# Optimization experiments

Measured on AMD Instinct MI355X. Metric: run time of the kernel, lower is better.

Reference implementation:

```python
import jax, jax.numpy as jnp
import numpy as np

N_NODES = 100000
N_EDGES = 800000
IN_SIZE = 256
OUT_SIZE = 256


def setup_inputs() -> dict:
    key = jax.random.key(0)
    k1, k2, k3, k4, k5, k6 = jax.random.split(key, 6)
    stdv = 1.0 / np.sqrt(OUT_SIZE)
    x = jax.random.normal(k1, (N_NODES, IN_SIZE), dtype=jnp.float32)
    weight = jax.random.uniform(k2, (IN_SIZE, OUT_SIZE), dtype=jnp.float32, minval=-stdv, maxval=stdv)
    bias = jax.random.uniform(k3, (1, OUT_SIZE), dtype=jnp.float32, minval=-stdv, maxval=stdv)
    edge_weight = jax.random.uniform(k4, (N_EDGES,), dtype=jnp.float32)
    edge_src = jax.random.randint(k5, (N_EDGES,), 0, N_NODES, dtype=jnp.int32)
    edge_dst = jax.random.randint(k6, (N_EDGES,), 0, N_NODES, dtype=jnp.int32)
    return {"x": x, "weight": weight, "bias": bias,
            "edge_weight": edge_weight, "edge_src": edge_src, "edge_dst": edge_dst}


def reference(x, weight, bias, edge_weight, edge_src, edge_dst):
    # supp = input @ W  (dense GEMM)
    supp = jnp.matmul(x, weight)  # [N, out]
    # out = spmm(A, supp): A in COO form -> gather source rows, scale, scatter-add to dst
    msgs = supp[edge_src] * edge_weight[:, None]  # [E, out]
    agg = jax.ops.segment_sum(msgs, edge_dst, num_segments=x.shape[0])  # [N, out]
    return agg + bias
```

## Files before the change

### kernel.cpp

```cpp
#include <hip/hip_runtime.h>
#include <hip/hip_bf16.h>

#define N_NODES 100000
#define N_EDGES 800000
#define K_DIM 256
#define N_DIM 256

typedef __attribute__((ext_vector_type(8)))  short  short8;
typedef __attribute__((ext_vector_type(4)))  float  f32x4;
typedef __attribute__((ext_vector_type(4)))  float  float4v;

__device__ short g_Wt[K_DIM * N_DIM];
__device__ int   g_bsums[512];
__device__ int   g_boff[512];

static __device__ inline short f32_to_bf16s(float f) {
    __bf16 h = (__bf16)f;
    return __builtin_bit_cast(short, h);
}

__global__ __launch_bounds__(256) void convert_w_kernel(const float* __restrict__ W) {
    const int n = blockIdx.x;
    const int k = threadIdx.x;
    g_Wt[n * K_DIM + k] = f32_to_bf16s(W[(size_t)k * N_DIM + n]);
}

__global__ __launch_bounds__(256) void mfma_gemm_kernel(const float* __restrict__ X,
                                                        float* __restrict__ S,
                                                        int M) {
    const int wave = threadIdx.x >> 6;
    const int lane = threadIdx.x & 63;
    const int r    = lane & 15;
    const int kg   = lane >> 4;
    const int m0   = blockIdx.x * 64;
    const int wc   = wave * 64;

    f32x4 acc[4][4];
    #pragma unroll
    for (int i = 0; i < 4; ++i)
        #pragma unroll
        for (int j = 0; j < 4; ++j)
            acc[i][j] = (f32x4)0.f;

    #pragma unroll
    for (int k0 = 0; k0 < K_DIM; k0 += 32) {
        short8 a[4], b[4];
        #pragma unroll
        for (int mi = 0; mi < 4; ++mi) {
            int row = m0 + mi * 16 + r;
            row = row < M ? row : (M - 1);
            const float* p = X + (size_t)row * K_DIM + k0 + kg * 8;
            float4v lo = *reinterpret_cast<const float4v*>(p);
            float4v hi = *reinterpret_cast<const float4v*>(p + 4);
            short8 v;
            v[0] = f32_to_bf16s(lo[0]); v[1] = f32_to_bf16s(lo[1]);
            v[2] = f32_to_bf16s(lo[2]); v[3] = f32_to_bf16s(lo[3]);
            v[4] = f32_to_bf16s(hi[0]); v[5] = f32_to_bf16s(hi[1]);
            v[6] = f32_to_bf16s(hi[2]); v[7] = f32_to_bf16s(hi[3]);
            a[mi] = v;
        }
        #pragma unroll
        for (int ni = 0; ni < 4; ++ni) {
            const short* q = g_Wt + (size_t)(wc + ni * 16 + r) * K_DIM + k0 + kg * 8;
            b[ni] = *reinterpret_cast<const short8*>(q);
        }
        #pragma unroll
        for (int mi = 0; mi < 4; ++mi)
            #pragma unroll
            for (int ni = 0; ni < 4; ++ni)
                acc[mi][ni] = __builtin_amdgcn_mfma_f32_16x16x32_bf16(a[mi], b[ni], acc[mi][ni], 0, 0, 0);
    }

    #pragma unroll
    for (int mi = 0; mi < 4; ++mi) {
        #pragma unroll
        for (int reg = 0; reg < 4; ++reg) {
            const int row = m0 + mi * 16 + kg * 4 + reg;
            if (row < M) {
                #pragma unroll
                for (int ni = 0; ni < 4; ++ni)
                    S[(size_t)row * N_DIM + wc + ni * 16 + r] = acc[mi][ni][reg];
            }
        }
    }
}

__global__ __launch_bounds__(256) void count_kernel(const int* __restrict__ edst,
                                                    int* __restrict__ counts, int E) {
    int e = blockIdx.x * 256 + threadIdx.x;
    if (e < E) atomicAdd(&counts[edst[e]], 1);
}

#define SCAN_NB ((N_NODES + 255) / 256)

__global__ __launch_bounds__(256) void scan1_kernel(const int* __restrict__ counts) {
    __shared__ int ws[4];
    const int i = blockIdx.x * 256 + threadIdx.x;
    int v = (i < N_NODES) ? counts[i] : 0;
    #pragma unroll
    for (int st = 32; st > 0; st >>= 1) v += __shfl_down(v, st, 64);
    if ((threadIdx.x & 63) == 0) ws[threadIdx.x >> 6] = v;
    __syncthreads();
    if (threadIdx.x == 0) g_bsums[blockIdx.x] = ws[0] + ws[1] + ws[2] + ws[3];
}

__global__ __launch_bounds__(512) void scan2_kernel() {
    __shared__ int s[512];
    const int t = threadIdx.x;
    int v = (t < SCAN_NB) ? g_bsums[t] : 0;
    s[t] = v;
    __syncthreads();
    for (int st = 1; st < 512; st <<= 1) {
        int u = (t >= st) ? s[t - st] : 0;
        __syncthreads();
        s[t] += u;
        __syncthreads();
    }
    g_boff[t] = s[t] - v;
}

__global__ __launch_bounds__(256) void scan3_kernel(const int* __restrict__ counts,
                                                    int* __restrict__ offsets) {
    __shared__ int s[256];
    const int t = threadIdx.x;
    const int i = blockIdx.x * 256 + t;
    int v = (i < N_NODES) ? counts[i] : 0;
    s[t] = v;
    __syncthreads();
    for (int st = 1; st < 256; st <<= 1) {
        int u = (t >= st) ? s[t - st] : 0;
        __syncthreads();
        s[t] += u;
        __syncthreads();
    }
    if (i < N_NODES) offsets[i + 1] = g_boff[blockIdx.x] + s[t];
    if (i == 0) offsets[0] = 0;
}

__global__ __launch_bounds__(256) void fill_kernel(const int* __restrict__ esrc,
                                                   const int* __restrict__ edst,
                                                   const float* __restrict__ ew,
                                                   const int* __restrict__ offsets,
                                                   int* __restrict__ cursor,
                                                   int2* __restrict__ csr, int E) {
    int e = blockIdx.x * 256 + threadIdx.x;
    if (e >= E) return;
    int d   = edst[e];
    int pos = offsets[d] + atomicAdd(&cursor[d], 1);
    csr[pos] = make_int2(esrc[e], __float_as_int(ew[e]));
}

__global__ __launch_bounds__(256) void gather_kernel(const float* __restrict__ S,
                                                     const float* __restrict__ bias,
                                                     const int* __restrict__ offsets,
                                                     const int2* __restrict__ csr,
                                                     float* __restrict__ out) {
    const int tid  = threadIdx.x;
    const int node = blockIdx.x * 4 + (tid >> 6);
    if (node >= N_NODES) return;
    const int lane = tid & 63;

    const int row = offsets[node];
    const int end = offsets[node + 1];

    float4v acc = *reinterpret_cast<const float4v*>(bias + lane * 4);

    int2 p = (row < end) ? csr[row] : make_int2(0, 0);
    for (int j = row; j < end; ++j) {
        const int2 pn = (j + 1 < end) ? csr[j + 1] : p;
        const float w = __int_as_float(p.y);
        const float4v v = *reinterpret_cast<const float4v*>(S + (size_t)p.x * N_DIM + lane * 4);
        acc += v * w;
        p = pn;
    }

    *reinterpret_cast<float4v*>(out + (size_t)node * N_DIM + lane * 4) = acc;
}

__global__ __launch_bounds__(256) void init_out_kernel(float* __restrict__ out,
                                                       const float* __restrict__ bias,
                                                       int total) {
    int i = blockIdx.x * 256 + threadIdx.x;
    if (i < total) out[i] = bias[i & (N_DIM - 1)];
}

__global__ __launch_bounds__(256) void scatter_kernel(const float* __restrict__ S,
                                                      const float* __restrict__ ew,
                                                      const int* __restrict__ esrc,
                                                      const int* __restrict__ edst,
                                                      float* __restrict__ out, int E) {
    const int tid  = threadIdx.x;
    const int e    = blockIdx.x * 4 + (tid >> 6);
    if (e >= E) return;
    const int lane = tid & 63;
    const int   s = esrc[e];
    const int   d = edst[e];
    const float w = ew[e];
    const float4v v = *reinterpret_cast<const float4v*>(S + (size_t)s * N_DIM + lane * 4);
    float* o = out + (size_t)d * N_DIM + lane * 4;
    unsafeAtomicAdd(o + 0, v[0] * w);
    unsafeAtomicAdd(o + 1, v[1] * w);
    unsafeAtomicAdd(o + 2, v[2] * w);
    unsafeAtomicAdd(o + 3, v[3] * w);
}

extern "C" void kernel_launch(void* const* d_in, const int* in_sizes, int n_in,
                              void* d_out, int out_size, void* d_ws, size_t ws_size,
                              hipStream_t stream) {
    const float* x      = (const float*)d_in[0];
    const float* weight = (const float*)d_in[1];
    const float* bias   = (const float*)d_in[2];
    const float* ew     = (const float*)d_in[3];
    const int*   esrc   = (const int*)d_in[4];
    const int*   edst   = (const int*)d_in[5];
    float*       out    = (float*)d_out;

    char*  ws     = (char*)d_ws;
    const size_t SUPP_B = (size_t)N_NODES * N_DIM * 4;
    const size_t CNT_B  = (size_t)N_NODES * 4;
    const size_t OFF_B  = ((size_t)(N_NODES + 1) * 4 + 15) & ~(size_t)15;
    const size_t CSR_B  = (size_t)N_EDGES * 8;

    float* supp    = (float*)(ws);
    int*   counts  = (int*)  (ws + SUPP_B);
    int*   cursor  = (int*)  (ws + SUPP_B + CNT_B);
    int*   offsets = (int*)  (ws + SUPP_B + 2 * CNT_B);
    int2*  csr     = (int2*) (ws + SUPP_B + 2 * CNT_B + OFF_B);
    const size_t NEEDED = SUPP_B + 2 * CNT_B + OFF_B + CSR_B;

    convert_w_kernel<<<N_DIM, 256, 0, stream>>>(weight);
    mfma_gemm_kernel<<<(N_NODES + 63) / 64, 256, 0, stream>>>(x, supp, N_NODES);

    if (ws_size >= NEEDED) {
        hipMemsetAsync(counts, 0, 2 * CNT_B, stream);
        count_kernel<<<(N_EDGES + 255) / 256, 256, 0, stream>>>(edst, counts, N_EDGES);
        scan1_kernel<<<SCAN_NB, 256, 0, stream>>>(counts);
        scan2_kernel<<<1, 512, 0, stream>>>();
        scan3_kernel<<<SCAN_NB, 256, 0, stream>>>(counts, offsets);
        fill_kernel<<<(N_EDGES + 255) / 256, 256, 0, stream>>>(esrc, edst, ew, offsets,
                                                               cursor, csr, N_EDGES);
        gather_kernel<<<(N_NODES + 3) / 4, 256, 0, stream>>>(supp, bias, offsets, csr, out);
    } else {
        int total = N_NODES * N_DIM;
        init_out_kernel<<<(total + 255) / 256, 256, 0, stream>>>(out, bias, total);
        scatter_kernel<<<(N_EDGES + 3) / 4, 256, 0, stream>>>(supp, ew, esrc, edst, out, N_EDGES);
    }
}
```

Baseline: 467.3 us.

## Store GEMM output as bf16 and unroll gather over edge pairs

```diff
diff --git a/kernel.cpp b/kernel.cpp
--- a/kernel.cpp
+++ b/kernel.cpp
@@ -6,9 +6,9 @@
 #define K_DIM 256
 #define N_DIM 256
 
-typedef __attribute__((ext_vector_type(8)))  short  short8;
+typedef __attribute__((ext_vector_type(8)))  short  bf16x8;
+typedef __attribute__((ext_vector_type(4)))  short  bf16x4;
 typedef __attribute__((ext_vector_type(4)))  float  f32x4;
-typedef __attribute__((ext_vector_type(4)))  float  float4v;
 
 __device__ short g_Wt[K_DIM * N_DIM];
 __device__ int   g_bsums[512];
@@ -17,6 +17,10 @@
 static __device__ inline short f32_to_bf16s(float f) {
     __bf16 h = (__bf16)f;
     return __builtin_bit_cast(short, h);
+}
+static __device__ inline float bf16s_to_f32(short s) {
+    unsigned int u = ((unsigned int)(unsigned short)s) << 16;
+    return __uint_as_float(u);
 }
 
 __global__ __launch_bounds__(256) void convert_w_kernel(const float* __restrict__ W) {
@@ -26,7 +30,7 @@
 }
 
 __global__ __launch_bounds__(256) void mfma_gemm_kernel(const float* __restrict__ X,
-                                                        float* __restrict__ S,
+                                                        short* __restrict__ Sb,
                                                         int M) {
     const int wave = threadIdx.x >> 6;
     const int lane = threadIdx.x & 63;
@@ -44,15 +48,15 @@
 
     #pragma unroll
     for (int k0 = 0; k0 < K_DIM; k0 += 32) {
-        short8 a[4], b[4];
+        bf16x8 a[4], b[4];
         #pragma unroll
         for (int mi = 0; mi < 4; ++mi) {
             int row = m0 + mi * 16 + r;
             row = row < M ? row : (M - 1);
             const float* p = X + (size_t)row * K_DIM + k0 + kg * 8;
-            float4v lo = *reinterpret_cast<const float4v*>(p);
-            float4v hi = *reinterpret_cast<const float4v*>(p + 4);
-            short8 v;
+            f32x4 lo = *reinterpret_cast<const f32x4*>(p);
+            f32x4 hi = *reinterpret_cast<const f32x4*>(p + 4);
+            bf16x8 v;
             v[0] = f32_to_bf16s(lo[0]); v[1] = f32_to_bf16s(lo[1]);
             v[2] = f32_to_bf16s(lo[2]); v[3] = f32_to_bf16s(lo[3]);
             v[4] = f32_to_bf16s(hi[0]); v[5] = f32_to_bf16s(hi[1]);
@@ -62,7 +66,7 @@
         #pragma unroll
         for (int ni = 0; ni < 4; ++ni) {
             const short* q = g_Wt + (size_t)(wc + ni * 16 + r) * K_DIM + k0 + kg * 8;
-            b[ni] = *reinterpret_cast<const short8*>(q);
+            b[ni] = *reinterpret_cast<const bf16x8*>(q);
         }
         #pragma unroll
         for (int mi = 0; mi < 4; ++mi)
@@ -79,7 +83,7 @@
             if (row < M) {
                 #pragma unroll
                 for (int ni = 0; ni < 4; ++ni)
-                    S[(size_t)row * N_DIM + wc + ni * 16 + r] = acc[mi][ni][reg];
+                    Sb[(size_t)row * N_DIM + wc + ni * 16 + r] = f32_to_bf16s(acc[mi][ni][reg]);
             }
         }
     }
@@ -94,14 +98,14 @@
 #define SCAN_NB ((N_NODES + 255) / 256)
 
 __global__ __launch_bounds__(256) void scan1_kernel(const int* __restrict__ counts) {
-    __shared__ int ws[4];
+    __shared__ int wsum[4];
     const int i = blockIdx.x * 256 + threadIdx.x;
     int v = (i < N_NODES) ? counts[i] : 0;
     #pragma unroll
     for (int st = 32; st > 0; st >>= 1) v += __shfl_down(v, st, 64);
-    if ((threadIdx.x & 63) == 0) ws[threadIdx.x >> 6] = v;
+    if ((threadIdx.x & 63) == 0) wsum[threadIdx.x >> 6] = v;
     __syncthreads();
-    if (threadIdx.x == 0) g_bsums[blockIdx.x] = ws[0] + ws[1] + ws[2] + ws[3];
+    if (threadIdx.x == 0) g_bsums[blockIdx.x] = wsum[0] + wsum[1] + wsum[2] + wsum[3];
 }
 
 __global__ __launch_bounds__(512) void scan2_kernel() {
@@ -120,7 +124,8 @@
 }
 
 __global__ __launch_bounds__(256) void scan3_kernel(const int* __restrict__ counts,
-                                                    int* __restrict__ offsets) {
+                                                    int* __restrict__ offsets,
+                                                    int* __restrict__ cursor) {
     __shared__ int s[256];
     const int t = threadIdx.x;
     const int i = blockIdx.x * 256 + t;
@@ -133,24 +138,26 @@
         s[t] += u;
         __syncthreads();
     }
-    if (i < N_NODES) offsets[i + 1] = g_boff[blockIdx.x] + s[t];
+    if (i < N_NODES) {
+        int inc = g_boff[blockIdx.x] + s[t];
+        offsets[i + 1] = inc;
+        cursor[i]      = inc - v;
+    }
     if (i == 0) offsets[0] = 0;
 }
 
 __global__ __launch_bounds__(256) void fill_kernel(const int* __restrict__ esrc,
                                                    const int* __restrict__ edst,
                                                    const float* __restrict__ ew,
-                                                   const int* __restrict__ offsets,
                                                    int* __restrict__ cursor,
                                                    int2* __restrict__ csr, int E) {
     int e = blockIdx.x * 256 + threadIdx.x;
     if (e >= E) return;
-    int d   = edst[e];
-    int pos = offsets[d] + atomicAdd(&cursor[d], 1);
+    int pos = atomicAdd(&cursor[edst[e]], 1);
     csr[pos] = make_int2(esrc[e], __float_as_int(ew[e]));
 }
 
-__global__ __launch_bounds__(256) void gather_kernel(const float* __restrict__ S,
+__global__ __launch_bounds__(256) void gather_kernel(const short* __restrict__ Sb,
                                                      const float* __restrict__ bias,
                                                      const int* __restrict__ offsets,
                                                      const int2* __restrict__ csr,
@@ -163,18 +170,30 @@
     const int row = offsets[node];
     const int end = offsets[node + 1];
 
-    float4v acc = *reinterpret_cast<const float4v*>(bias + lane * 4);
-
-    int2 p = (row < end) ? csr[row] : make_int2(0, 0);
-    for (int j = row; j < end; ++j) {
-        const int2 pn = (j + 1 < end) ? csr[j + 1] : p;
+    f32x4 acc = *reinterpret_cast<const f32x4*>(bias + lane * 4);
+
+    int j = row;
+    for (; j + 2 <= end; j += 2) {
+        const int2 p0 = csr[j];
+        const int2 p1 = csr[j + 1];
+        const bf16x4 v0 = *reinterpret_cast<const bf16x4*>(Sb + (size_t)p0.x * N_DIM + lane * 4);
+        const bf16x4 v1 = *reinterpret_cast<const bf16x4*>(Sb + (size_t)p1.x * N_DIM + lane * 4);
+        const float w0 = __int_as_float(p0.y);
+        const float w1 = __int_as_float(p1.y);
+        #pragma unroll
+        for (int c = 0; c < 4; ++c)
+            acc[c] += bf16s_to_f32(v0[c]) * w0 + bf16s_to_f32(v1[c]) * w1;
+    }
+    if (j < end) {
+        const int2 p = csr[j];
+        const bf16x4 v = *reinterpret_cast<const bf16x4*>(Sb + (size_t)p.x * N_DIM + lane * 4);
         const float w = __int_as_float(p.y);
-        const float4v v = *reinterpret_cast<const float4v*>(S + (size_t)p.x * N_DIM + lane * 4);
-        acc += v * w;
-        p = pn;
-    }
-
-    *reinterpret_cast<float4v*>(out + (size_t)node * N_DIM + lane * 4) = acc;
+        #pragma unroll
+        for (int c = 0; c < 4; ++c)
+            acc[c] += bf16s_to_f32(v[c]) * w;
+    }
+
+    *reinterpret_cast<f32x4*>(out + (size_t)node * N_DIM + lane * 4) = acc;
 }
 
 __global__ __launch_bounds__(256) void init_out_kernel(float* __restrict__ out,
@@ -184,7 +203,7 @@
     if (i < total) out[i] = bias[i & (N_DIM - 1)];
 }
 
-__global__ __launch_bounds__(256) void scatter_kernel(const float* __restrict__ S,
+__global__ __launch_bounds__(256) void scatter_kernel(const short* __restrict__ Sb,
                                                       const float* __restrict__ ew,
                                                       const int* __restrict__ esrc,
                                                       const int* __restrict__ edst,
@@ -196,12 +215,12 @@
     const int   s = esrc[e];
     const int   d = edst[e];
     const float w = ew[e];
-    const float4v v = *reinterpret_cast<const float4v*>(S + (size_t)s * N_DIM + lane * 4);
+    const bf16x4 v = *reinterpret_cast<const bf16x4*>(Sb + (size_t)s * N_DIM + lane * 4);
     float* o = out + (size_t)d * N_DIM + lane * 4;
-    unsafeAtomicAdd(o + 0, v[0] * w);
-    unsafeAtomicAdd(o + 1, v[1] * w);
-    unsafeAtomicAdd(o + 2, v[2] * w);
-    unsafeAtomicAdd(o + 3, v[3] * w);
+    unsafeAtomicAdd(o + 0, bf16s_to_f32(v[0]) * w);
+    unsafeAtomicAdd(o + 1, bf16s_to_f32(v[1]) * w);
+    unsafeAtomicAdd(o + 2, bf16s_to_f32(v[2]) * w);
+    unsafeAtomicAdd(o + 3, bf16s_to_f32(v[3]) * w);
 }
 
 extern "C" void kernel_launch(void* const* d_in, const int* in_sizes, int n_in,
@@ -216,12 +235,12 @@
     float*       out    = (float*)d_out;
 
     char*  ws     = (char*)d_ws;
-    const size_t SUPP_B = (size_t)N_NODES * N_DIM * 4;
+    const size_t SUPP_B = ((size_t)N_NODES * N_DIM * 2 + 255) & ~(size_t)255;
     const size_t CNT_B  = (size_t)N_NODES * 4;
     const size_t OFF_B  = ((size_t)(N_NODES + 1) * 4 + 15) & ~(size_t)15;
     const size_t CSR_B  = (size_t)N_EDGES * 8;
 
-    float* supp    = (float*)(ws);
+    short* supp    = (short*)(ws);
     int*   counts  = (int*)  (ws + SUPP_B);
     int*   cursor  = (int*)  (ws + SUPP_B + CNT_B);
     int*   offsets = (int*)  (ws + SUPP_B + 2 * CNT_B);
@@ -232,12 +251,12 @@
     mfma_gemm_kernel<<<(N_NODES + 63) / 64, 256, 0, stream>>>(x, supp, N_NODES);
 
     if (ws_size >= NEEDED) {
-        hipMemsetAsync(counts, 0, 2 * CNT_B, stream);
+        (void)hipMemsetAsync(counts, 0, CNT_B, stream);
         count_kernel<<<(N_EDGES + 255) / 256, 256, 0, stream>>>(edst, counts, N_EDGES);
         scan1_kernel<<<SCAN_NB, 256, 0, stream>>>(counts);
         scan2_kernel<<<1, 512, 0, stream>>>();
-        scan3_kernel<<<SCAN_NB, 256, 0, stream>>>(counts, offsets);
-        fill_kernel<<<(N_EDGES + 255) / 256, 256, 0, stream>>>(esrc, edst, ew, offsets,
+        scan3_kernel<<<SCAN_NB, 256, 0, stream>>>(counts, offsets, cursor);
+        fill_kernel<<<(N_EDGES + 255) / 256, 256, 0, stream>>>(esrc, edst, ew,
                                                                cursor, csr, N_EDGES);
         gather_kernel<<<(N_NODES + 3) / 4, 256, 0, stream>>>(supp, bias, offsets, csr, out);
     } else {
```

New measurement: 414.1 us. 11.4% less time.
